# Kernel optimization log

Measured on AMD Instinct MI355X. Metric: run time of the kernel, lower is better.

Reference implementation:

```python
import jax, jax.numpy as jnp
import numpy as np

N_NODES = 10000
N_EDGES = 160000
MUL0 = 128   # multiplicity of 0e in node input/output
MUL1 = 64    # multiplicity of 1o in node input/output
FC_IN = 8    # radial basis size (edge_scalar_attr dim)
FC_H = 64    # fc_neurons = [64, 64]
NUM_NEIGHBORS = 16.0
ANGLE = np.pi / 8.0
MID0 = MUL0 + MUL1   # 192 scalars in irreps_mid (simplified)
MID1 = MUL0 + MUL1   # 192 vectors (1o) in irreps_mid


def _inv_sqrt(d):
    return 1.0 / np.sqrt(d)


def setup_inputs() -> dict:
    key = jax.random.key(0)
    ks = jax.random.split(key, 18)
    rn = lambda k, shape: jax.random.normal(k, shape, dtype=jnp.float32)
    inp = {
        'node_input': rn(ks[0], (N_NODES, MUL0 + 3 * MUL1)),
        'edge_attr': rn(ks[1], (N_EDGES, 4)),            # 1x0e + 1x1o spherical harmonics
        'edge_scalar_attr': rn(ks[2], (N_EDGES, FC_IN)),
        # first Linear: node_input -> (node_features || node_self_out)
        'Wa0': rn(ks[3], (MUL0, MUL0)),   # 0e -> 0e (message branch)
        'Wa1': rn(ks[4], (MUL1, MUL1)),   # 1o -> 1o (message branch)
        'Wb0': rn(ks[5], (MUL0, MUL0)),   # 0e -> 0e (self branch)
        'Wb1': rn(ks[6], (MUL1, MUL1)),   # 1o -> 1o (self branch)
        # radial MLP
        'M1': rn(ks[7], (FC_IN, FC_H)),
        'M2': rn(ks[8], (FC_H, FC_H)),
        # per-instruction TP weight generators: [FC_H, mul] ('uvu', v=1 squeezed)
        'Wtp0': rn(ks[9], (FC_H, MUL0)),   # 0e x 0e -> 0e
        'Wtp1': rn(ks[10], (FC_H, MUL0)),  # 0e x 1o -> 1o
        'Wtp2': rn(ks[11], (FC_H, MUL1)),  # 1o x 0e -> 1o
        'Wtp3': rn(ks[12], (FC_H, MUL1)),  # 1o x 1o -> 0e
        # output Linear: irreps_mid (192x0e + 192x1o) -> 128x0e + 64x1o
        'Wo0': rn(ks[13], (MID0, MUL0)),
        'Wo1': rn(ks[14], (MID1, MUL1)),
        'edge_src': jax.random.randint(ks[15], (N_EDGES,), 0, N_NODES),
        'edge_dst': jax.random.randint(ks[16], (N_EDGES,), 0, N_NODES),
    }
    return inp


def _forward(node_input, edge_attr, edge_scalar_attr,
             Wa0, Wa1, Wb0, Wb1, M1, M2,
             Wtp0, Wtp1, Wtp2, Wtp3, Wo0, Wo1,
             edge_src, edge_dst):
    n = node_input.shape[0]
    x0 = node_input[:, :MUL0]                         # [N,128] 0e
    x1 = node_input[:, MUL0:].reshape(n, MUL1, 3)     # [N,64,3] 1o

    # Linear(node_input.irreps + irreps_node_output): split into message / self
    feat0 = (x0 @ Wa0) * _inv_sqrt(MUL0)
    feat1 = jnp.einsum('nvi,vu->nui', x1, Wa1) * _inv_sqrt(MUL1)
    self0 = (x0 @ Wb0) * _inv_sqrt(MUL0)
    self1 = jnp.einsum('nvi,vu->nui', x1, Wb1) * _inv_sqrt(MUL1)

    # gather node features to edges
    e0 = feat0[edge_src]                              # [E,128]
    e1 = feat1[edge_src]                              # [E,64,3]
    y0 = edge_attr[:, 0:1]                            # [E,1] 0e
    y1 = edge_attr[:, 1:4]                            # [E,3] 1o

    # radial MLP -> per-edge per-path 'uvu' weights (path param / sqrt(fc_out))
    h = jax.nn.gelu(edge_scalar_attr @ M1 * _inv_sqrt(FC_IN))
    h = jax.nn.gelu(h @ M2 * _inv_sqrt(FC_H))
    w0 = h @ Wtp0 * _inv_sqrt(FC_H)                   # [E,128]
    w1 = h @ Wtp1 * _inv_sqrt(FC_H)                   # [E,128]
    w2 = h @ Wtp2 * _inv_sqrt(FC_H)                   # [E,64]
    w3 = h @ Wtp3 * _inv_sqrt(FC_H)                   # [E,64]

    # CG tensor product paths (component normalization: alpha = sqrt(dim_out))
    mid0a = w0 * e0 * y0                                        # 0e x 0e -> 0e [E,128]
    mid0b = w3 * jnp.einsum('eui,ei->eu', e1, y1) * _inv_sqrt(3.0)  # 1o.1o -> 0e [E,64]
    mid1a = w1[:, :, None] * e0[:, :, None] * y1[:, None, :]   # 0e x 1o -> 1o [E,128,3]
    mid1b = w2[:, :, None] * e1 * y0[:, :, None]                # 1o x 0e -> 1o [E,64,3]

    e_cnt = edge_attr.shape[0]
    edge_mid = jnp.concatenate(
        [mid0a, mid0b, mid1a.reshape(e_cnt, -1), mid1b.reshape(e_cnt, -1)], axis=1)  # [E,768]

    # scatter-add to destination nodes, divide by sqrt(num_neighbors)
    agg = jax.ops.segment_sum(edge_mid, edge_dst, num_segments=n) * _inv_sqrt(NUM_NEIGHBORS)

    z0 = agg[:, :MID0]                                          # [N,192] 0e
    z1 = jnp.concatenate(
        [agg[:, MID0:MID0 + 3 * MUL0].reshape(n, MUL0, 3),
         agg[:, MID0 + 3 * MUL0:].reshape(n, MUL1, 3)], axis=1)  # [N,192,3] 1o

    conv0 = (z0 @ Wo0) * _inv_sqrt(MID0)
    conv1 = jnp.einsum('nvi,vu->nui', z1, Wo1) * _inv_sqrt(MID1)

    c = np.cos(ANGLE).astype(np.float32)
    s = np.sin(ANGLE).astype(np.float32)
    out0 = c * self0 + s * conv0                                 # [N,128]
    out1 = c * self1 + s * conv1                                 # [N,64,3]
    return jnp.concatenate([out0, out1.reshape(n, -1)], axis=1)  # [N,320]


def reference(node_input, edge_attr, edge_scalar_attr,
              Wa0, Wa1, Wb0, Wb1, M1, M2,
              Wtp0, Wtp1, Wtp2, Wtp3, Wo0, Wo1,
              edge_src, edge_dst):
    return _forward(node_input, edge_attr, edge_scalar_attr,
                    Wa0, Wa1, Wb0, Wb1, M1, M2,
                    Wtp0, Wtp1, Wtp2, Wtp3, Wo0, Wo1,
                    edge_src, edge_dst)
```

## Files before the change

### kernel.cpp

```cpp
#include <hip/hip_runtime.h>
#include <hip/hip_bf16.h>
#include <hip/hip_fp16.h>

#define N_NODES 10000
#define N_EDGES 160000
#define FEAT_W 320
#define CHUNK 32

typedef _Float16 half8 __attribute__((ext_vector_type(8)));
typedef float f32x4 __attribute__((ext_vector_type(4)));

__device__ __forceinline__ float gelu_tanh(float x) {
    float x3 = x * x * x;
    float t = tanhf(0.7978845608028654f * (x + 0.044715f * x3));
    return 0.5f * x * (1.0f + t);
}

__global__ __launch_bounds__(320) void node_transform(
    const float* __restrict__ node_input,
    const float* __restrict__ Wa0, const float* __restrict__ Wa1,
    const float* __restrict__ Wb0, const float* __restrict__ Wb1,
    float* __restrict__ feat_tbl, float* __restrict__ self_tbl)
{
    __shared__ __align__(16) float xT[FEAT_W][8];
    const int node0 = blockIdx.x * 8;
    const int t = threadIdx.x;
    for (int q = t; q < 640; q += 320) {
        const int n = q / 80, c4 = q - n * 80;
        const float4 v = ((const float4*)(node_input + (size_t)(node0 + n) * FEAT_W))[c4];
        xT[c4 * 4 + 0][n] = v.x; xT[c4 * 4 + 1][n] = v.y;
        xT[c4 * 4 + 2][n] = v.z; xT[c4 * 4 + 3][n] = v.w;
    }
    __syncthreads();

    float accf[8] = {0,0,0,0,0,0,0,0}, accs[8] = {0,0,0,0,0,0,0,0};
    float scale;
    if (t < 128) {
        for (int v = 0; v < 128; ++v) {
            const float wa = Wa0[v * 128 + t];
            const float wb = Wb0[v * 128 + t];
            const float4 xa = *(const float4*)&xT[v][0];
            const float4 xb = *(const float4*)&xT[v][4];
            accf[0] += xa.x * wa; accf[1] += xa.y * wa; accf[2] += xa.z * wa; accf[3] += xa.w * wa;
            accf[4] += xb.x * wa; accf[5] += xb.y * wa; accf[6] += xb.z * wa; accf[7] += xb.w * wa;
            accs[0] += xa.x * wb; accs[1] += xa.y * wb; accs[2] += xa.z * wb; accs[3] += xa.w * wb;
            accs[4] += xb.x * wb; accs[5] += xb.y * wb; accs[6] += xb.z * wb; accs[7] += xb.w * wb;
        }
        scale = 0.08838834764831845f;
    } else {
        const int r = t - 128, u = r / 3, i = r - 3 * u;
        for (int v = 0; v < 64; ++v) {
            const float wa = Wa1[v * 64 + u];
            const float wb = Wb1[v * 64 + u];
            const int row = 128 + v * 3 + i;
            const float4 xa = *(const float4*)&xT[row][0];
            const float4 xb = *(const float4*)&xT[row][4];
            accf[0] += xa.x * wa; accf[1] += xa.y * wa; accf[2] += xa.z * wa; accf[3] += xa.w * wa;
            accf[4] += xb.x * wa; accf[5] += xb.y * wa; accf[6] += xb.z * wa; accf[7] += xb.w * wa;
            accs[0] += xa.x * wb; accs[1] += xa.y * wb; accs[2] += xa.z * wb; accs[3] += xa.w * wb;
            accs[4] += xb.x * wb; accs[5] += xb.y * wb; accs[6] += xb.z * wb; accs[7] += xb.w * wb;
        }
        scale = 0.125f;
    }
#pragma unroll
    for (int n = 0; n < 8; ++n) {
        feat_tbl[(size_t)(node0 + n) * FEAT_W + t] = accf[n] * scale;
        self_tbl[(size_t)(node0 + n) * FEAT_W + t] = accs[n] * scale;
    }
}

__global__ __launch_bounds__(256) void count_kernel(
    const int* __restrict__ edge_dst, int* __restrict__ counts)
{
    const int e = blockIdx.x * 256 + threadIdx.x;
    if (e < N_EDGES) atomicAdd(&counts[edge_dst[e]], 1);
}

__global__ __launch_bounds__(1024) void scan_kernel(
    const int* __restrict__ counts, int* __restrict__ offsets, int* __restrict__ cursor)
{
    __shared__ int wsum[16];
    const int wid = threadIdx.x >> 6, lane = threadIdx.x & 63;
    int base = 0;
    for (int c = 0; c < 10; ++c) {
        const int i = c * 1024 + threadIdx.x;
        const int v = (i < N_NODES) ? counts[i] : 0;
        int x = v;
#pragma unroll
        for (int off = 1; off < 64; off <<= 1) {
            int y = __shfl_up(x, off, 64);
            if (lane >= off) x += y;
        }
        if (lane == 63) wsum[wid] = x;
        __syncthreads();
        if (threadIdx.x < 16) {
            int s = wsum[threadIdx.x];
#pragma unroll
            for (int off = 1; off < 16; off <<= 1) {
                int y = __shfl_up(s, off, 64);
                if ((int)threadIdx.x >= off) s += y;
            }
            wsum[threadIdx.x] = s;
        }
        __syncthreads();
        const int waveoff = (wid == 0) ? 0 : wsum[wid - 1];
        const int excl = base + waveoff + x - v;
        if (i < N_NODES) { offsets[i] = excl; cursor[i] = excl; }
        const int tot = wsum[15];
        __syncthreads();
        base += tot;
    }
    if (threadIdx.x == 0) offsets[N_NODES] = base;
}

__global__ void fill_kernel(const int* __restrict__ edge_dst,
                            const int* __restrict__ edge_src,
                            const float* __restrict__ edge_attr,
                            int* __restrict__ cursor,
                            int* __restrict__ srcs_csr, float* __restrict__ y4csr,
                            int* __restrict__ pos_csr) {
    int e = blockIdx.x * 256 + threadIdx.x;
    if (e < N_EDGES) {
        int pos = atomicAdd(&cursor[edge_dst[e]], 1);
        srcs_csr[pos] = edge_src[e];
        ((float4*)y4csr)[pos] = ((const float4*)edge_attr)[e];
        pos_csr[e] = pos;
    }
}

__global__ __launch_bounds__(256) void mlp_kernel(
    const float* __restrict__ esa,
    const float* __restrict__ M1,
    const float* __restrict__ M2,
    const int* __restrict__ pos_csr,
    __half* __restrict__ h2csr)
{
    __shared__ __align__(16) float sh[4][64];
    const int wave = threadIdx.x >> 6;
    const int lane = threadIdx.x & 63;
    const int e = blockIdx.x * 4 + wave;

    const int pos = pos_csr[e];

    const float4 e0 = ((const float4*)(esa + (size_t)e * 8))[0];
    const float4 e1 = ((const float4*)(esa + (size_t)e * 8))[1];
    float h = e0.x * M1[0 * 64 + lane] + e0.y * M1[1 * 64 + lane]
            + e0.z * M1[2 * 64 + lane] + e0.w * M1[3 * 64 + lane]
            + e1.x * M1[4 * 64 + lane] + e1.y * M1[5 * 64 + lane]
            + e1.z * M1[6 * 64 + lane] + e1.w * M1[7 * 64 + lane];
    h = gelu_tanh(h * 0.35355339059327373f);
    sh[wave][lane] = h;
    __syncthreads();

    float h2 = 0.f;
    const float4* shp = (const float4*)sh[wave];
#pragma unroll
    for (int q = 0; q < 16; ++q) {
        const float4 s = shp[q];
        h2 += s.x * M2[(4 * q + 0) * 64 + lane];
        h2 += s.y * M2[(4 * q + 1) * 64 + lane];
        h2 += s.z * M2[(4 * q + 2) * 64 + lane];
        h2 += s.w * M2[(4 * q + 3) * 64 + lane];
    }
    h2 = gelu_tanh(h2 * 0.125f);
    h2csr[(size_t)pos * 64 + lane] = (__half)(h2 * 0.125f);
}

__global__ __launch_bounds__(256) void pack_weights(
    const float* __restrict__ Wtp0, const float* __restrict__ Wtp1,
    const float* __restrict__ Wtp2, const float* __restrict__ Wtp3,
    const float* __restrict__ Wo0,  const float* __restrict__ Wo1,
    __half* __restrict__ wtp_pack, __half* __restrict__ wo_pack)
{
    const int gid = blockIdx.x * 256 + threadIdx.x;
    if (gid < 1536) {
        const int lane = gid & 63;
        const int tile = gid >> 6;
        const int quad = lane >> 4, n16 = lane & 15;
        const int col = tile * 16 + n16;
        const float* src; int stride;
        if (col < 128)      { src = Wtp0 + col;         stride = 128; }
        else if (col < 256) { src = Wtp1 + (col - 128); stride = 128; }
        else if (col < 320) { src = Wtp2 + (col - 256); stride = 64;  }
        else                { src = Wtp3 + (col - 320); stride = 64;  }
        __half* dst = wtp_pack + (size_t)gid * 16;
#pragma unroll
        for (int s = 0; s < 2; ++s)
#pragma unroll
            for (int j = 0; j < 8; ++j)
                dst[s * 8 + j] = (__half)src[(s * 32 + quad * 8 + j) * stride];
    } else {
        const int i = gid - 1536;
        if (i < 24576) wo_pack[i] = (__half)Wo0[i];
        else           wo_pack[i] = (__half)Wo1[i - 24576];
    }
}

__global__ __launch_bounds__(384, 4) void gather_kernel(
    const int* __restrict__ offsets,
    const int* __restrict__ srcs_csr,
    const float* __restrict__ y4csr,
    const __half* __restrict__ h2csr,
    const __half* __restrict__ wtp_pack,
    const float* __restrict__ feat_tbl,
    const float* __restrict__ self_tbl,
    const __half* __restrict__ wo_pack,
    float* __restrict__ out)
{
    __shared__ __align__(16) __half wsh[CHUNK * 384];
    __shared__ __align__(16) char pool[CHUNK * 128];
    __shared__ float ys[CHUNK][4];
    __shared__ int   srcs[CHUNK];
    __half* h2s = (__half*)pool;
    float*  z   = (float*)pool;

    const int node = blockIdx.x;
    const int t = threadIdx.x;
    const int wave = t >> 6, lane = t & 63;
    const int quad = lane >> 4, n16 = lane & 15;

    const int beg = offsets[node], end = offsets[node + 1];

    int cb = beg;
    int ne = min(CHUNK, end - cb);
    half8 hreg = {};
    int   sreg = 0;
    float4 yreg = {0.f, 0.f, 0.f, 0.f};
    if (t < ne * 8) hreg = ((const half8*)(h2csr + (size_t)cb * 64))[t];
    if (t < ne)     { sreg = srcs_csr[cb + t]; yreg = ((const float4*)y4csr)[cb + t]; }

    half8 bf[4][2];
#pragma unroll
    for (int c = 0; c < 4; ++c) {
        const __half* p = wtp_pack + (size_t)((wave * 4 + c) * 64 + lane) * 16;
        bf[c][0] = *(const half8*)p;
        bf[c][1] = *(const half8*)(p + 8);
    }

    int f0;
    if (t < 128)      f0 = t;
    else if (t < 256) f0 = t - 128;
    else if (t < 320) f0 = 128 + 3 * (t - 256);
    else              f0 = 128 + 3 * (t - 320);

    float acc = 0.f, acc3a = 0.f, acc3b = 0.f, acc3c = 0.f;

    for (;;) {
        if (t < ne) { srcs[t] = sreg; ((float4*)ys)[t] = yreg; }
        if (t < ne * 8) {
            const int eL = t >> 3, u = t & 7;
            *(half8*)((char*)h2s + eL * 128 + ((u * 16) ^ ((eL & 7) << 4))) = hreg;
        }
        __syncthreads();

#pragma unroll
        for (int g = 0; g < 2; ++g) {
            if (g * 16 < ne) {
                const int e = g * 16 + n16;
                const char* hb = (const char*)h2s + e * 128;
                const int sw = (e & 7) << 4;
                const half8 af0 = *(const half8*)(hb + ((quad * 16) ^ sw));
                const half8 af1 = *(const half8*)(hb + ((64 + quad * 16) ^ sw));
#pragma unroll
                for (int c = 0; c < 4; ++c) {
                    f32x4 acc4 = {0.f, 0.f, 0.f, 0.f};
                    acc4 = __builtin_amdgcn_mfma_f32_16x16x32_f16(af0, bf[c][0], acc4, 0, 0, 0);
                    acc4 = __builtin_amdgcn_mfma_f32_16x16x32_f16(af1, bf[c][1], acc4, 0, 0, 0);
                    const int colb = ((wave * 4 + c) * 16 + n16) * 2;
#pragma unroll
                    for (int r = 0; r < 4; ++r) {
                        const int row = g * 16 + quad * 4 + r;
                        *(__half*)((char*)wsh + row * 768 + (colb ^ (quad << 5))) =
                            (__half)acc4[r];
                    }
                }
            }
        }

        const int cb2 = cb + CHUNK;
        const int ne2 = (cb2 < end) ? min(CHUNK, end - cb2) : 0;
        if (t < ne2 * 8) hreg = ((const half8*)(h2csr + (size_t)cb2 * 64))[t];
        if (t < ne2)     { sreg = srcs_csr[cb2 + t]; yreg = ((const float4*)y4csr)[cb2 + t]; }
        __syncthreads();

        const int tb = t * 2;
#define WRD(ee) __half2float(*(const __half*)((const char*)wsh + (ee) * 768 + (tb ^ ((((ee) >> 2) & 3) << 5))))
        if (t < 128) {
            int e = 0;
            for (; e + 4 <= ne; e += 4) {
                float w4[4], v4[4]; int s4[4];
#pragma unroll
                for (int k = 0; k < 4; ++k) { w4[k] = WRD(e + k); s4[k] = srcs[e + k]; }
#pragma unroll
                for (int k = 0; k < 4; ++k) v4[k] = feat_tbl[(size_t)s4[k] * FEAT_W + f0];
#pragma unroll
                for (int k = 0; k < 4; ++k) acc += w4[k] * v4[k] * ys[e + k][0];
            }
            for (; e < ne; ++e)
                acc += WRD(e) * feat_tbl[(size_t)srcs[e] * FEAT_W + f0] * ys[e][0];
        } else if (t < 256) {
            int e = 0;
            for (; e + 4 <= ne; e += 4) {
                float w4[4], v4[4]; int s4[4];
#pragma unroll
                for (int k = 0; k < 4; ++k) { w4[k] = WRD(e + k); s4[k] = srcs[e + k]; }
#pragma unroll
                for (int k = 0; k < 4; ++k) v4[k] = feat_tbl[(size_t)s4[k] * FEAT_W + f0];
#pragma unroll
                for (int k = 0; k < 4; ++k) {
                    const float p = w4[k] * v4[k];
                    a3aAdd: ;
                    acc3a += p * ys[e + k][1];
                    acc3b += p * ys[e + k][2];
                    acc3c += p * ys[e + k][3];
                }
            }
            for (; e < ne; ++e) {
                const float p = WRD(e) * feat_tbl[(size_t)srcs[e] * FEAT_W + f0];
                acc3a += p * ys[e][1]; acc3b += p * ys[e][2]; acc3c += p * ys[e][3];
            }
        } else if (t < 320) {
            int e = 0;
            for (; e + 4 <= ne; e += 4) {
                float w4[4], va[4], vb[4], vc[4]; int s4[4];
#pragma unroll
                for (int k = 0; k < 4; ++k) { w4[k] = WRD(e + k); s4[k] = srcs[e + k]; }
#pragma unroll
                for (int k = 0; k < 4; ++k) {
                    const float* fr = feat_tbl + (size_t)s4[k] * FEAT_W;
                    va[k] = fr[f0]; vb[k] = fr[f0 + 1]; vc[k] = fr[f0 + 2];
                }
#pragma unroll
                for (int k = 0; k < 4; ++k) {
                    const float p = w4[k] * ys[e + k][0];
                    acc3a += p * va[k]; acc3b += p * vb[k]; acc3c += p * vc[k];
                }
            }
            for (; e < ne; ++e) {
                const float* fr = feat_tbl + (size_t)srcs[e] * FEAT_W;
                const float p = WRD(e) * ys[e][0];
                acc3a += p * fr[f0]; acc3b += p * fr[f0 + 1]; acc3c += p * fr[f0 + 2];
            }
        } else {
            int e = 0;
            for (; e + 4 <= ne; e += 4) {
                float w4[4], va[4], vb[4], vc[4]; int s4[4];
#pragma unroll
                for (int k = 0; k < 4; ++k) { w4[k] = WRD(e + k); s4[k] = srcs[e + k]; }
#pragma unroll
                for (int k = 0; k < 4; ++k) {
                    const float* fr = feat_tbl + (size_t)s4[k] * FEAT_W;
                    va[k] = fr[f0]; vb[k] = fr[f0 + 1]; vc[k] = fr[f0 + 2];
                }
#pragma unroll
                for (int k = 0; k < 4; ++k)
                    acc += w4[k] * (va[k] * ys[e + k][1] + vb[k] * ys[e + k][2]
                                  + vc[k] * ys[e + k][3]);
            }
            for (; e < ne; ++e) {
                const float* fr = feat_tbl + (size_t)srcs[e] * FEAT_W;
                acc += WRD(e) * (fr[f0] * ys[e][1] + fr[f0 + 1] * ys[e][2]
                               + fr[f0 + 2] * ys[e][3]);
            }
        }
#undef WRD

        if (!ne2) break;
        cb = cb2; ne = ne2;
        __syncthreads();
    }

    const float sZ = 0.25f;
    if (t < 128) {
        z[t] = acc * sZ;
    } else if (t < 256) {
        const int u = t - 128;
        z[192 + 0 * 192 + u] = acc3a * sZ;
        z[192 + 1 * 192 + u] = acc3b * sZ;
        z[192 + 2 * 192 + u] = acc3c * sZ;
    } else if (t < 320) {
        const int u = t - 256;
        z[192 + 0 * 192 + 128 + u] = acc3a * sZ;
        z[192 + 1 * 192 + 128 + u] = acc3b * sZ;
        z[192 + 2 * 192 + 128 + u] = acc3c * sZ;
    } else {
        z[128 + (t - 320)] = acc * sZ * 0.5773502691896258f;
    }
    __syncthreads();

    const float sA = 0.07216878364870323f;
    const float cR = 0.92387953251128674f;
    const float sR = 0.38268343236508978f;
    const __half* Wo0h = wo_pack;
    const __half* Wo1h = wo_pack + 24576;

    if (t < 128) {
        float conv = 0.f;
        const float4* z4 = (const float4*)z;
#pragma unroll 8
        for (int q = 0; q < 48; ++q) {
            const float4 zz = z4[q];
            conv += zz.x * (float)Wo0h[(4 * q + 0) * 128 + t];
            conv += zz.y * (float)Wo0h[(4 * q + 1) * 128 + t];
            conv += zz.z * (float)Wo0h[(4 * q + 2) * 128 + t];
            conv += zz.w * (float)Wo0h[(4 * q + 3) * 128 + t];
        }
        const float sv = self_tbl[(size_t)node * FEAT_W + t];
        out[(size_t)node * FEAT_W + t] = cR * sv + sR * conv * sA;
    } else if (t < 320) {
        const int idx = t - 128;
        const int i = idx >> 6, u = idx & 63;
        float conv = 0.f;
        const float4* z4 = (const float4*)(z + 192 + i * 192);
#pragma unroll 8
        for (int q = 0; q < 48; ++q) {
            const float4 zz = z4[q];
            conv += zz.x * (float)Wo1h[(4 * q + 0) * 64 + u];
            conv += zz.y * (float)Wo1h[(4 * q + 1) * 64 + u];
            conv += zz.z * (float)Wo1h[(4 * q + 2) * 64 + u];
            conv += zz.w * (float)Wo1h[(4 * q + 3) * 64 + u];
        }
        const int col = 128 + u * 3 + i;
        const float sv = self_tbl[(size_t)node * FEAT_W + col];
        out[(size_t)node * FEAT_W + col] = cR * sv + sR * conv * sA;
    }
}

extern "C" void kernel_launch(void* const* d_in, const int* in_sizes, int n_in,
                              void* d_out, int out_size, void* d_ws, size_t ws_size,
                              hipStream_t stream) {
    const float* node_input = (const float*)d_in[0];
    const float* edge_attr  = (const float*)d_in[1];
    const float* esa        = (const float*)d_in[2];
    const float* Wa0  = (const float*)d_in[3];
    const float* Wa1  = (const float*)d_in[4];
    const float* Wb0  = (const float*)d_in[5];
    const float* Wb1  = (const float*)d_in[6];
    const float* M1   = (const float*)d_in[7];
    const float* M2   = (const float*)d_in[8];
    const float* Wtp0 = (const float*)d_in[9];
    const float* Wtp1 = (const float*)d_in[10];
    const float* Wtp2 = (const float*)d_in[11];
    const float* Wtp3 = (const float*)d_in[12];
    const float* Wo0  = (const float*)d_in[13];
    const float* Wo1  = (const float*)d_in[14];
    const int* edge_src = (const int*)d_in[15];
    const int* edge_dst = (const int*)d_in[16];
    float* out = (float*)d_out;

    char* w = (char*)d_ws;
    float*  feat_tbl = (float*)w;           w += (size_t)N_NODES * FEAT_W * 4;
    float*  self_tbl = (float*)w;           w += (size_t)N_NODES * FEAT_W * 4;
    float*  y4csr    = (float*)w;           w += (size_t)N_EDGES * 4 * 4;
    __half* h2csr    = (__half*)w;          w += (size_t)N_EDGES * 64 * 2;
    __half* wtp_pack = (__half*)w;          w += (size_t)24576 * 2;
    __half* wo_pack  = (__half*)w;          w += (size_t)36864 * 2;
    int*    counts   = (int*)w;             w += (size_t)N_NODES * 4;
    int*    offsets  = (int*)w;             w += (size_t)(N_NODES + 1) * 4;
    int*    cursor   = (int*)w;             w += (size_t)N_NODES * 4;
    int*    srcs_csr = (int*)w;             w += (size_t)N_EDGES * 4;
    int*    pos_csr  = (int*)w;             w += (size_t)N_EDGES * 4;

    hipMemsetAsync(counts, 0, sizeof(int) * N_NODES, stream);

    count_kernel<<<N_EDGES / 256, 256, 0, stream>>>(edge_dst, counts);
    scan_kernel<<<1, 1024, 0, stream>>>(counts, offsets, cursor);
    fill_kernel<<<N_EDGES / 256, 256, 0, stream>>>(edge_dst, edge_src, edge_attr,
                                                   cursor, srcs_csr, y4csr, pos_csr);
    pack_weights<<<150, 256, 0, stream>>>(Wtp0, Wtp1, Wtp2, Wtp3, Wo0, Wo1,
                                          wtp_pack, wo_pack);
    node_transform<<<N_NODES / 8, 320, 0, stream>>>(node_input, Wa0, Wa1, Wb0, Wb1,
                                                    feat_tbl, self_tbl);
    mlp_kernel<<<N_EDGES / 4, 256, 0, stream>>>(esa, M1, M2, pos_csr, h2csr);
    gather_kernel<<<N_NODES, 384, 0, stream>>>(offsets, srcs_csr, y4csr, h2csr,
                                               wtp_pack, feat_tbl, self_tbl,
                                               wo_pack, out);
}
```

Before: 402.5 us.

## Merge prep kernels, fold CSR fill into MLP, persistent gather grid

Node transform, edge counting and weight packing are fused into one launch, with edges recording their atomic rank so CSR positions come from offsets plus rank. This removes the fill kernel and the cursor array. The MLP kernel now scatters src and edge_attr itself and uses 512-thread blocks. Gather becomes a grid-stride loop over nodes with 1280 blocks, and the GELU tanh is replaced by an exp-based formula. Together these reduce launch count and serial dependency stages, at the cost of more complex kernels and possible load imbalance in the persistent gather loop.

```diff
diff --git a/kernel.cpp b/kernel.cpp
--- a/kernel.cpp
+++ b/kernel.cpp
@@ -6,78 +6,108 @@
 #define N_EDGES 160000
 #define FEAT_W 320
 #define CHUNK 32
+#define GATHER_GRID 1280
 
 typedef _Float16 half8 __attribute__((ext_vector_type(8)));
 typedef float f32x4 __attribute__((ext_vector_type(4)));
 
 __device__ __forceinline__ float gelu_tanh(float x) {
     float x3 = x * x * x;
-    float t = tanhf(0.7978845608028654f * (x + 0.044715f * x3));
-    return 0.5f * x * (1.0f + t);
-}
-
-__global__ __launch_bounds__(320) void node_transform(
+    float y = 0.7978845608028654f * (x + 0.044715f * x3);
+    float th = 1.f - 2.f / (__expf(2.f * y) + 1.f);
+    return 0.5f * x * (1.f + th);
+}
+
+__global__ __launch_bounds__(320) void prep_kernel(
     const float* __restrict__ node_input,
     const float* __restrict__ Wa0, const float* __restrict__ Wa1,
     const float* __restrict__ Wb0, const float* __restrict__ Wb1,
-    float* __restrict__ feat_tbl, float* __restrict__ self_tbl)
+    float* __restrict__ feat_tbl, float* __restrict__ self_tbl,
+    const int* __restrict__ edge_dst, int* __restrict__ counts,
+    int* __restrict__ rank,
+    const float* __restrict__ Wtp0, const float* __restrict__ Wtp1,
+    const float* __restrict__ Wtp2, const float* __restrict__ Wtp3,
+    const float* __restrict__ Wo0,  const float* __restrict__ Wo1,
+    __half* __restrict__ wtp_pack, __half* __restrict__ wo_pack)
 {
     __shared__ __align__(16) float xT[FEAT_W][8];
-    const int node0 = blockIdx.x * 8;
     const int t = threadIdx.x;
-    for (int q = t; q < 640; q += 320) {
-        const int n = q / 80, c4 = q - n * 80;
-        const float4 v = ((const float4*)(node_input + (size_t)(node0 + n) * FEAT_W))[c4];
-        xT[c4 * 4 + 0][n] = v.x; xT[c4 * 4 + 1][n] = v.y;
-        xT[c4 * 4 + 2][n] = v.z; xT[c4 * 4 + 3][n] = v.w;
-    }
-    __syncthreads();
-
-    float accf[8] = {0,0,0,0,0,0,0,0}, accs[8] = {0,0,0,0,0,0,0,0};
-    float scale;
-    if (t < 128) {
-        for (int v = 0; v < 128; ++v) {
-            const float wa = Wa0[v * 128 + t];
-            const float wb = Wb0[v * 128 + t];
-            const float4 xa = *(const float4*)&xT[v][0];
-            const float4 xb = *(const float4*)&xT[v][4];
-            accf[0] += xa.x * wa; accf[1] += xa.y * wa; accf[2] += xa.z * wa; accf[3] += xa.w * wa;
-            accf[4] += xb.x * wa; accf[5] += xb.y * wa; accf[6] += xb.z * wa; accf[7] += xb.w * wa;
-            accs[0] += xa.x * wb; accs[1] += xa.y * wb; accs[2] += xa.z * wb; accs[3] += xa.w * wb;
-            accs[4] += xb.x * wb; accs[5] += xb.y * wb; accs[6] += xb.z * wb; accs[7] += xb.w * wb;
-        }
-        scale = 0.08838834764831845f;
+
+    if (blockIdx.x < 1250) {
+        const int node0 = blockIdx.x * 8;
+        for (int q = t; q < 640; q += 320) {
+            const int n = q / 80, c4 = q - n * 80;
+            const float4 v = ((const float4*)(node_input + (size_t)(node0 + n) * FEAT_W))[c4];
+            xT[c4 * 4 + 0][n] = v.x; xT[c4 * 4 + 1][n] = v.y;
+            xT[c4 * 4 + 2][n] = v.z; xT[c4 * 4 + 3][n] = v.w;
+        }
+        __syncthreads();
+
+        float accf[8] = {0,0,0,0,0,0,0,0}, accs[8] = {0,0,0,0,0,0,0,0};
+        float scale;
+        if (t < 128) {
+            for (int v = 0; v < 128; ++v) {
+                const float wa = Wa0[v * 128 + t];
+                const float wb = Wb0[v * 128 + t];
+                const float4 xa = *(const float4*)&xT[v][0];
+                const float4 xb = *(const float4*)&xT[v][4];
+                accf[0] += xa.x * wa; accf[1] += xa.y * wa; accf[2] += xa.z * wa; accf[3] += xa.w * wa;
+                accf[4] += xb.x * wa; accf[5] += xb.y * wa; accf[6] += xb.z * wa; accf[7] += xb.w * wa;
+                accs[0] += xa.x * wb; accs[1] += xa.y * wb; accs[2] += xa.z * wb; accs[3] += xa.w * wb;
+                accs[4] += xb.x * wb; accs[5] += xb.y * wb; accs[6] += xb.z * wb; accs[7] += xb.w * wb;
+            }
+            scale = 0.08838834764831845f;
+        } else {
+            const int r = t - 128, u = r / 3, i = r - 3 * u;
+            for (int v = 0; v < 64; ++v) {
+                const float wa = Wa1[v * 64 + u];
+                const float wb = Wb1[v * 64 + u];
+                const int row = 128 + v * 3 + i;
+                const float4 xa = *(const float4*)&xT[row][0];
+                const float4 xb = *(const float4*)&xT[row][4];
+                accf[0] += xa.x * wa; accf[1] += xa.y * wa; accf[2] += xa.z * wa; accf[3] += xa.w * wa;
+                accf[4] += xb.x * wa; accf[5] += xb.y * wa; accf[6] += xb.z * wa; accf[7] += xb.w * wa;
+                accs[0] += xa.x * wb; accs[1] += xa.y * wb; accs[2] += xa.z * wb; accs[3] += xa.w * wb;
+                accs[4] += xb.x * wb; accs[5] += xb.y * wb; accs[6] += xb.z * wb; accs[7] += xb.w * wb;
+            }
+            scale = 0.125f;
+        }
+#pragma unroll
+        for (int n = 0; n < 8; ++n) {
+            feat_tbl[(size_t)(node0 + n) * FEAT_W + t] = accf[n] * scale;
+            self_tbl[(size_t)(node0 + n) * FEAT_W + t] = accs[n] * scale;
+        }
+    } else if (blockIdx.x < 1750) {
+        const int e = (blockIdx.x - 1250) * 320 + t;
+        rank[e] = atomicAdd(&counts[edge_dst[e]], 1);
     } else {
-        const int r = t - 128, u = r / 3, i = r - 3 * u;
-        for (int v = 0; v < 64; ++v) {
-            const float wa = Wa1[v * 64 + u];
-            const float wb = Wb1[v * 64 + u];
-            const int row = 128 + v * 3 + i;
-            const float4 xa = *(const float4*)&xT[row][0];
-            const float4 xb = *(const float4*)&xT[row][4];
-            accf[0] += xa.x * wa; accf[1] += xa.y * wa; accf[2] += xa.z * wa; accf[3] += xa.w * wa;
-            accf[4] += xb.x * wa; accf[5] += xb.y * wa; accf[6] += xb.z * wa; accf[7] += xb.w * wa;
-            accs[0] += xa.x * wb; accs[1] += xa.y * wb; accs[2] += xa.z * wb; accs[3] += xa.w * wb;
-            accs[4] += xb.x * wb; accs[5] += xb.y * wb; accs[6] += xb.z * wb; accs[7] += xb.w * wb;
-        }
-        scale = 0.125f;
-    }
-#pragma unroll
-    for (int n = 0; n < 8; ++n) {
-        feat_tbl[(size_t)(node0 + n) * FEAT_W + t] = accf[n] * scale;
-        self_tbl[(size_t)(node0 + n) * FEAT_W + t] = accs[n] * scale;
-    }
-}
-
-__global__ __launch_bounds__(256) void count_kernel(
-    const int* __restrict__ edge_dst, int* __restrict__ counts)
-{
-    const int e = blockIdx.x * 256 + threadIdx.x;
-    if (e < N_EDGES) atomicAdd(&counts[edge_dst[e]], 1);
+        const int gid = (blockIdx.x - 1750) * 320 + t;
+        if (gid < 1536) {
+            const int lane = gid & 63;
+            const int tile = gid >> 6;
+            const int quad = lane >> 4, n16 = lane & 15;
+            const int col = tile * 16 + n16;
+            const float* src; int stride;
+            if (col < 128)      { src = Wtp0 + col;         stride = 128; }
+            else if (col < 256) { src = Wtp1 + (col - 128); stride = 128; }
+            else if (col < 320) { src = Wtp2 + (col - 256); stride = 64;  }
+            else                { src = Wtp3 + (col - 320); stride = 64;  }
+            __half* dst = wtp_pack + (size_t)gid * 16;
+#pragma unroll
+            for (int s = 0; s < 2; ++s)
+#pragma unroll
+                for (int j = 0; j < 8; ++j)
+                    dst[s * 8 + j] = (__half)src[(s * 32 + quad * 8 + j) * stride];
+        } else if (gid < 38400) {
+            const int i = gid - 1536;
+            if (i < 24576) wo_pack[i] = (__half)Wo0[i];
+            else           wo_pack[i] = (__half)Wo1[i - 24576];
+        }
+    }
 }
 
 __global__ __launch_bounds__(1024) void scan_kernel(
-    const int* __restrict__ counts, int* __restrict__ offsets, int* __restrict__ cursor)
+    const int* __restrict__ counts, int* __restrict__ offsets)
 {
     __shared__ int wsum[16];
     const int wid = threadIdx.x >> 6, lane = threadIdx.x & 63;
@@ -105,7 +135,7 @@
         __syncthreads();
         const int waveoff = (wid == 0) ? 0 : wsum[wid - 1];
         const int excl = base + waveoff + x - v;
-        if (i < N_NODES) { offsets[i] = excl; cursor[i] = excl; }
+        if (i < N_NODES) offsets[i] = excl;
         const int tot = wsum[15];
         __syncthreads();
         base += tot;
@@ -113,34 +143,29 @@
     if (threadIdx.x == 0) offsets[N_NODES] = base;
 }
 
-__global__ void fill_kernel(const int* __restrict__ edge_dst,
-                            const int* __restrict__ edge_src,
-                            const float* __restrict__ edge_attr,
-                            int* __restrict__ cursor,
-                            int* __restrict__ srcs_csr, float* __restrict__ y4csr,
-                            int* __restrict__ pos_csr) {
-    int e = blockIdx.x * 256 + threadIdx.x;
-    if (e < N_EDGES) {
-        int pos = atomicAdd(&cursor[edge_dst[e]], 1);
-        srcs_csr[pos] = edge_src[e];
-        ((float4*)y4csr)[pos] = ((const float4*)edge_attr)[e];
-        pos_csr[e] = pos;
-    }
-}
-
-__global__ __launch_bounds__(256) void mlp_kernel(
+__global__ __launch_bounds__(512) void mlp_kernel(
     const float* __restrict__ esa,
     const float* __restrict__ M1,
     const float* __restrict__ M2,
-    const int* __restrict__ pos_csr,
-    __half* __restrict__ h2csr)
+    const int* __restrict__ edge_dst,
+    const int* __restrict__ rank,
+    const int* __restrict__ offsets,
+    const int* __restrict__ edge_src,
+    const float* __restrict__ edge_attr,
+    __half* __restrict__ h2csr,
+    int* __restrict__ srcs_csr,
+    float* __restrict__ y4csr)
 {
-    __shared__ __align__(16) float sh[4][64];
+    __shared__ __align__(16) float sh[8][64];
     const int wave = threadIdx.x >> 6;
     const int lane = threadIdx.x & 63;
-    const int e = blockIdx.x * 4 + wave;
-
-    const int pos = pos_csr[e];
+    const int e = blockIdx.x * 8 + wave;
+
+    const int pos = offsets[edge_dst[e]] + rank[e];
+    if (lane == 0) {
+        srcs_csr[pos] = edge_src[e];
+        ((float4*)y4csr)[pos] = ((const float4*)edge_attr)[e];
+    }
 
     const float4 e0 = ((const float4*)(esa + (size_t)e * 8))[0];
     const float4 e1 = ((const float4*)(esa + (size_t)e * 8))[1];
@@ -164,36 +189,6 @@
     }
     h2 = gelu_tanh(h2 * 0.125f);
     h2csr[(size_t)pos * 64 + lane] = (__half)(h2 * 0.125f);
-}
-
-__global__ __launch_bounds__(256) void pack_weights(
-    const float* __restrict__ Wtp0, const float* __restrict__ Wtp1,
-    const float* __restrict__ Wtp2, const float* __restrict__ Wtp3,
-    const float* __restrict__ Wo0,  const float* __restrict__ Wo1,
-    __half* __restrict__ wtp_pack, __half* __restrict__ wo_pack)
-{
-    const int gid = blockIdx.x * 256 + threadIdx.x;
-    if (gid < 1536) {
-        const int lane = gid & 63;
-        const int tile = gid >> 6;
-        const int quad = lane >> 4, n16 = lane & 15;
-        const int col = tile * 16 + n16;
-        const float* src; int stride;
-        if (col < 128)      { src = Wtp0 + col;         stride = 128; }
-        else if (col < 256) { src = Wtp1 + (col - 128); stride = 128; }
-        else if (col < 320) { src = Wtp2 + (col - 256); stride = 64;  }
-        else                { src = Wtp3 + (col - 320); stride = 64;  }
-        __half* dst = wtp_pack + (size_t)gid * 16;
-#pragma unroll
-        for (int s = 0; s < 2; ++s)
-#pragma unroll
-            for (int j = 0; j < 8; ++j)
-                dst[s * 8 + j] = (__half)src[(s * 32 + quad * 8 + j) * stride];
-    } else {
-        const int i = gid - 1536;
-        if (i < 24576) wo_pack[i] = (__half)Wo0[i];
-        else           wo_pack[i] = (__half)Wo1[i - 24576];
-    }
 }
 
 __global__ __launch_bounds__(384, 4) void gather_kernel(
@@ -214,20 +209,9 @@
     __half* h2s = (__half*)pool;
     float*  z   = (float*)pool;
 
-    const int node = blockIdx.x;
     const int t = threadIdx.x;
     const int wave = t >> 6, lane = t & 63;
     const int quad = lane >> 4, n16 = lane & 15;
-
-    const int beg = offsets[node], end = offsets[node + 1];
-
-    int cb = beg;
-    int ne = min(CHUNK, end - cb);
-    half8 hreg = {};
-    int   sreg = 0;
-    float4 yreg = {0.f, 0.f, 0.f, 0.f};
-    if (t < ne * 8) hreg = ((const half8*)(h2csr + (size_t)cb * 64))[t];
-    if (t < ne)     { sreg = srcs_csr[cb + t]; yreg = ((const float4*)y4csr)[cb + t]; }
 
     half8 bf[4][2];
 #pragma unroll
@@ -236,193 +220,204 @@
         bf[c][0] = *(const half8*)p;
         bf[c][1] = *(const half8*)(p + 8);
     }
-
     int f0;
     if (t < 128)      f0 = t;
     else if (t < 256) f0 = t - 128;
     else if (t < 320) f0 = 128 + 3 * (t - 256);
     else              f0 = 128 + 3 * (t - 320);
 
-    float acc = 0.f, acc3a = 0.f, acc3b = 0.f, acc3c = 0.f;
-
-    for (;;) {
-        if (t < ne) { srcs[t] = sreg; ((float4*)ys)[t] = yreg; }
-        if (t < ne * 8) {
-            const int eL = t >> 3, u = t & 7;
-            *(half8*)((char*)h2s + eL * 128 + ((u * 16) ^ ((eL & 7) << 4))) = hreg;
-        }
-        __syncthreads();
-
-#pragma unroll
-        for (int g = 0; g < 2; ++g) {
-            if (g * 16 < ne) {
-                const int e = g * 16 + n16;
-                const char* hb = (const char*)h2s + e * 128;
-                const int sw = (e & 7) << 4;
-                const half8 af0 = *(const half8*)(hb + ((quad * 16) ^ sw));
-                const half8 af1 = *(const half8*)(hb + ((64 + quad * 16) ^ sw));
-#pragma unroll
-                for (int c = 0; c < 4; ++c) {
-                    f32x4 acc4 = {0.f, 0.f, 0.f, 0.f};
-                    acc4 = __builtin_amdgcn_mfma_f32_16x16x32_f16(af0, bf[c][0], acc4, 0, 0, 0);
-                    acc4 = __builtin_amdgcn_mfma_f32_16x16x32_f16(af1, bf[c][1], acc4, 0, 0, 0);
-                    const int colb = ((wave * 4 + c) * 16 + n16) * 2;
-#pragma unroll
-                    for (int r = 0; r < 4; ++r) {
-                        const int row = g * 16 + quad * 4 + r;
-                        *(__half*)((char*)wsh + row * 768 + (colb ^ (quad << 5))) =
-                            (__half)acc4[r];
-                    }
-                }
-            }
-        }
-
-        const int cb2 = cb + CHUNK;
-        const int ne2 = (cb2 < end) ? min(CHUNK, end - cb2) : 0;
-        if (t < ne2 * 8) hreg = ((const half8*)(h2csr + (size_t)cb2 * 64))[t];
-        if (t < ne2)     { sreg = srcs_csr[cb2 + t]; yreg = ((const float4*)y4csr)[cb2 + t]; }
-        __syncthreads();
-
-        const int tb = t * 2;
-#define WRD(ee) __half2float(*(const __half*)((const char*)wsh + (ee) * 768 + (tb ^ ((((ee) >> 2) & 3) << 5))))
-        if (t < 128) {
-            int e = 0;
-            for (; e + 4 <= ne; e += 4) {
-                float w4[4], v4[4]; int s4[4];
-#pragma unroll
-                for (int k = 0; k < 4; ++k) { w4[k] = WRD(e + k); s4[k] = srcs[e + k]; }
-#pragma unroll
-                for (int k = 0; k < 4; ++k) v4[k] = feat_tbl[(size_t)s4[k] * FEAT_W + f0];
-#pragma unroll
-                for (int k = 0; k < 4; ++k) acc += w4[k] * v4[k] * ys[e + k][0];
-            }
-            for (; e < ne; ++e)
-                acc += WRD(e) * feat_tbl[(size_t)srcs[e] * FEAT_W + f0] * ys[e][0];
-        } else if (t < 256) {
-            int e = 0;
-            for (; e + 4 <= ne; e += 4) {
-                float w4[4], v4[4]; int s4[4];
-#pragma unroll
-                for (int k = 0; k < 4; ++k) { w4[k] = WRD(e + k); s4[k] = srcs[e + k]; }
-#pragma unroll
-                for (int k = 0; k < 4; ++k) v4[k] = feat_tbl[(size_t)s4[k] * FEAT_W + f0];
-#pragma unroll
-                for (int k = 0; k < 4; ++k) {
-                    const float p = w4[k] * v4[k];
-                    a3aAdd: ;
-                    acc3a += p * ys[e + k][1];
-                    acc3b += p * ys[e + k][2];
-                    acc3c += p * ys[e + k][3];
-                }
-            }
-            for (; e < ne; ++e) {
-                const float p = WRD(e) * feat_tbl[(size_t)srcs[e] * FEAT_W + f0];
-                acc3a += p * ys[e][1]; acc3b += p * ys[e][2]; acc3c += p * ys[e][3];
-            }
-        } else if (t < 320) {
-            int e = 0;
-            for (; e + 4 <= ne; e += 4) {
-                float w4[4], va[4], vb[4], vc[4]; int s4[4];
-#pragma unroll
-                for (int k = 0; k < 4; ++k) { w4[k] = WRD(e + k); s4[k] = srcs[e + k]; }
-#pragma unroll
-                for (int k = 0; k < 4; ++k) {
-                    const float* fr = feat_tbl + (size_t)s4[k] * FEAT_W;
-                    va[k] = fr[f0]; vb[k] = fr[f0 + 1]; vc[k] = fr[f0 + 2];
-                }
-#pragma unroll
-                for (int k = 0; k < 4; ++k) {
-                    const float p = w4[k] * ys[e + k][0];
-                    acc3a += p * va[k]; acc3b += p * vb[k]; acc3c += p * vc[k];
-                }
-            }
-            for (; e < ne; ++e) {
-                const float* fr = feat_tbl + (size_t)srcs[e] * FEAT_W;
-                const float p = WRD(e) * ys[e][0];
-                acc3a += p * fr[f0]; acc3b += p * fr[f0 + 1]; acc3c += p * fr[f0 + 2];
-            }
-        } else {
-            int e = 0;
-            for (; e + 4 <= ne; e += 4) {
-                float w4[4], va[4], vb[4], vc[4]; int s4[4];
-#pragma unroll
-                for (int k = 0; k < 4; ++k) { w4[k] = WRD(e + k); s4[k] = srcs[e + k]; }
-#pragma unroll
-                for (int k = 0; k < 4; ++k) {
-                    const float* fr = feat_tbl + (size_t)s4[k] * FEAT_W;
-                    va[k] = fr[f0]; vb[k] = fr[f0 + 1]; vc[k] = fr[f0 + 2];
-                }
-#pragma unroll
-                for (int k = 0; k < 4; ++k)
-                    acc += w4[k] * (va[k] * ys[e + k][1] + vb[k] * ys[e + k][2]
-                                  + vc[k] * ys[e + k][3]);
-            }
-            for (; e < ne; ++e) {
-                const float* fr = feat_tbl + (size_t)srcs[e] * FEAT_W;
-                acc += WRD(e) * (fr[f0] * ys[e][1] + fr[f0 + 1] * ys[e][2]
-                               + fr[f0 + 2] * ys[e][3]);
-            }
-        }
-#undef WRD
-
-        if (!ne2) break;
-        cb = cb2; ne = ne2;
-        __syncthreads();
-    }
-
     const float sZ = 0.25f;
-    if (t < 128) {
-        z[t] = acc * sZ;
-    } else if (t < 256) {
-        const int u = t - 128;
-        z[192 + 0 * 192 + u] = acc3a * sZ;
-        z[192 + 1 * 192 + u] = acc3b * sZ;
-        z[192 + 2 * 192 + u] = acc3c * sZ;
-    } else if (t < 320) {
-        const int u = t - 256;
-        z[192 + 0 * 192 + 128 + u] = acc3a * sZ;
-        z[192 + 1 * 192 + 128 + u] = acc3b * sZ;
-        z[192 + 2 * 192 + 128 + u] = acc3c * sZ;
-    } else {
-        z[128 + (t - 320)] = acc * sZ * 0.5773502691896258f;
-    }
-    __syncthreads();
-
     const float sA = 0.07216878364870323f;
     const float cR = 0.92387953251128674f;
     const float sR = 0.38268343236508978f;
     const __half* Wo0h = wo_pack;
     const __half* Wo1h = wo_pack + 24576;
 
-    if (t < 128) {
-        float conv = 0.f;
-        const float4* z4 = (const float4*)z;
+    for (int node = blockIdx.x; node < N_NODES; node += GATHER_GRID) {
+        const int beg = offsets[node], end = offsets[node + 1];
+
+        int cb = beg;
+        int ne = min(CHUNK, end - cb);
+        half8 hreg = {};
+        int   sreg = 0;
+        float4 yreg = {0.f, 0.f, 0.f, 0.f};
+        if (t < ne * 8) hreg = ((const half8*)(h2csr + (size_t)cb * 64))[t];
+        if (t < ne)     { sreg = srcs_csr[cb + t]; yreg = ((const float4*)y4csr)[cb + t]; }
+
+        float acc = 0.f, acc3a = 0.f, acc3b = 0.f, acc3c = 0.f;
+
+        for (;;) {
+            if (t < ne) { srcs[t] = sreg; ((float4*)ys)[t] = yreg; }
+            if (t < ne * 8) {
+                const int eL = t >> 3, u = t & 7;
+                *(half8*)((char*)h2s + eL * 128 + ((u * 16) ^ ((eL & 7) << 4))) = hreg;
+            }
+            __syncthreads();
+
+#pragma unroll
+            for (int g = 0; g < 2; ++g) {
+                if (g * 16 < ne) {
+                    const int e = g * 16 + n16;
+                    const char* hb = (const char*)h2s + e * 128;
+                    const int sw = (e & 7) << 4;
+                    const half8 af0 = *(const half8*)(hb + ((quad * 16) ^ sw));
+                    const half8 af1 = *(const half8*)(hb + ((64 + quad * 16) ^ sw));
+#pragma unroll
+                    for (int c = 0; c < 4; ++c) {
+                        f32x4 acc4 = {0.f, 0.f, 0.f, 0.f};
+                        acc4 = __builtin_amdgcn_mfma_f32_16x16x32_f16(af0, bf[c][0], acc4, 0, 0, 0);
+                        acc4 = __builtin_amdgcn_mfma_f32_16x16x32_f16(af1, bf[c][1], acc4, 0, 0, 0);
+                        const int colb = ((wave * 4 + c) * 16 + n16) * 2;
+#pragma unroll
+                        for (int r = 0; r < 4; ++r) {
+                            const int row = g * 16 + quad * 4 + r;
+                            *(__half*)((char*)wsh + row * 768 + (colb ^ (quad << 5))) =
+                                (__half)acc4[r];
+                        }
+                    }
+                }
+            }
+
+            const int cb2 = cb + CHUNK;
+            const int ne2 = (cb2 < end) ? min(CHUNK, end - cb2) : 0;
+            if (t < ne2 * 8) hreg = ((const half8*)(h2csr + (size_t)cb2 * 64))[t];
+            if (t < ne2)     { sreg = srcs_csr[cb2 + t]; yreg = ((const float4*)y4csr)[cb2 + t]; }
+            __syncthreads();
+
+            const int tb = t * 2;
+#define WRD(ee) __half2float(*(const __half*)((const char*)wsh + (ee) * 768 + (tb ^ ((((ee) >> 2) & 3) << 5))))
+            if (t < 128) {
+                int e = 0;
+                for (; e + 4 <= ne; e += 4) {
+                    float w4[4], v4[4]; int s4[4];
+#pragma unroll
+                    for (int k = 0; k < 4; ++k) { w4[k] = WRD(e + k); s4[k] = srcs[e + k]; }
+#pragma unroll
+                    for (int k = 0; k < 4; ++k) v4[k] = feat_tbl[(size_t)s4[k] * FEAT_W + f0];
+#pragma unroll
+                    for (int k = 0; k < 4; ++k) acc += w4[k] * v4[k] * ys[e + k][0];
+                }
+                for (; e < ne; ++e)
+                    acc += WRD(e) * feat_tbl[(size_t)srcs[e] * FEAT_W + f0] * ys[e][0];
+            } else if (t < 256) {
+                int e = 0;
+                for (; e + 4 <= ne; e += 4) {
+                    float w4[4], v4[4]; int s4[4];
+#pragma unroll
+                    for (int k = 0; k < 4; ++k) { w4[k] = WRD(e + k); s4[k] = srcs[e + k]; }
+#pragma unroll
+                    for (int k = 0; k < 4; ++k) v4[k] = feat_tbl[(size_t)s4[k] * FEAT_W + f0];
+#pragma unroll
+                    for (int k = 0; k < 4; ++k) {
+                        const float p = w4[k] * v4[k];
+                        acc3a += p * ys[e + k][1];
+                        acc3b += p * ys[e + k][2];
+                        acc3c += p * ys[e + k][3];
+                    }
+                }
+                for (; e < ne; ++e) {
+                    const float p = WRD(e) * feat_tbl[(size_t)srcs[e] * FEAT_W + f0];
+                    acc3a += p * ys[e][1]; acc3b += p * ys[e][2]; acc3c += p * ys[e][3];
+                }
+            } else if (t < 320) {
+                int e = 0;
+                for (; e + 4 <= ne; e += 4) {
+                    float w4[4], va[4], vb[4], vc[4]; int s4[4];
+#pragma unroll
+                    for (int k = 0; k < 4; ++k) { w4[k] = WRD(e + k); s4[k] = srcs[e + k]; }
+#pragma unroll
+                    for (int k = 0; k < 4; ++k) {
+                        const float* fr = feat_tbl + (size_t)s4[k] * FEAT_W;
+                        va[k] = fr[f0]; vb[k] = fr[f0 + 1]; vc[k] = fr[f0 + 2];
+                    }
+#pragma unroll
+                    for (int k = 0; k < 4; ++k) {
+                        const float p = w4[k] * ys[e + k][0];
+                        acc3a += p * va[k]; acc3b += p * vb[k]; acc3c += p * vc[k];
+                    }
+                }
+                for (; e < ne; ++e) {
+                    const float* fr = feat_tbl + (size_t)srcs[e] * FEAT_W;
+                    const float p = WRD(e) * ys[e][0];
+                    acc3a += p * fr[f0]; acc3b += p * fr[f0 + 1]; acc3c += p * fr[f0 + 2];
+                }
+            } else {
+                int e = 0;
+                for (; e + 4 <= ne; e += 4) {
+                    float w4[4], va[4], vb[4], vc[4]; int s4[4];
+#pragma unroll
+                    for (int k = 0; k < 4; ++k) { w4[k] = WRD(e + k); s4[k] = srcs[e + k]; }
+#pragma unroll
+                    for (int k = 0; k < 4; ++k) {
+                        const float* fr = feat_tbl + (size_t)s4[k] * FEAT_W;
+                        va[k] = fr[f0]; vb[k] = fr[f0 + 1]; vc[k] = fr[f0 + 2];
+                    }
+#pragma unroll
+                    for (int k = 0; k < 4; ++k)
+                        acc += w4[k] * (va[k] * ys[e + k][1] + vb[k] * ys[e + k][2]
+                                      + vc[k] * ys[e + k][3]);
+                }
+                for (; e < ne; ++e) {
+                    const float* fr = feat_tbl + (size_t)srcs[e] * FEAT_W;
+                    acc += WRD(e) * (fr[f0] * ys[e][1] + fr[f0 + 1] * ys[e][2]
+                                   + fr[f0 + 2] * ys[e][3]);
+                }
+            }
+#undef WRD
+
+            if (!ne2) break;
+            cb = cb2; ne = ne2;
+            __syncthreads();
+        }
+
+        if (t < 128) {
+            z[t] = acc * sZ;
+        } else if (t < 256) {
+            const int u = t - 128;
+            z[192 + 0 * 192 + u] = acc3a * sZ;
+            z[192 + 1 * 192 + u] = acc3b * sZ;
+            z[192 + 2 * 192 + u] = acc3c * sZ;
+        } else if (t < 320) {
+            const int u = t - 256;
+            z[192 + 0 * 192 + 128 + u] = acc3a * sZ;
+            z[192 + 1 * 192 + 128 + u] = acc3b * sZ;
+            z[192 + 2 * 192 + 128 + u] = acc3c * sZ;
+        } else {
+            z[128 + (t - 320)] = acc * sZ * 0.5773502691896258f;
+        }
+        __syncthreads();
+
+        if (t < 128) {
+            float conv = 0.f;
+            const float4* z4 = (const float4*)z;
 #pragma unroll 8
-        for (int q = 0; q < 48; ++q) {
-            const float4 zz = z4[q];
-            conv += zz.x * (float)Wo0h[(4 * q + 0) * 128 + t];
-            conv += zz.y * (float)Wo0h[(4 * q + 1) * 128 + t];
-            conv += zz.z * (float)Wo0h[(4 * q + 2) * 128 + t];
-            conv += zz.w * (float)Wo0h[(4 * q + 3) * 128 + t];
-        }
-        const float sv = self_tbl[(size_t)node * FEAT_W + t];
-        out[(size_t)node * FEAT_W + t] = cR * sv + sR * conv * sA;
-    } else if (t < 320) {
-        const int idx = t - 128;
-        const int i = idx >> 6, u = idx & 63;
-        float conv = 0.f;
-        const float4* z4 = (const float4*)(z + 192 + i * 192);
+            for (int q = 0; q < 48; ++q) {
+                const float4 zz = z4[q];
+                conv += zz.x * (float)Wo0h[(4 * q + 0) * 128 + t];
+                conv += zz.y * (float)Wo0h[(4 * q + 1) * 128 + t];
+                conv += zz.z * (float)Wo0h[(4 * q + 2) * 128 + t];
+                conv += zz.w * (float)Wo0h[(4 * q + 3) * 128 + t];
+            }
+            const float sv = self_tbl[(size_t)node * FEAT_W + t];
+            out[(size_t)node * FEAT_W + t] = cR * sv + sR * conv * sA;
+        } else if (t < 320) {
+            const int idx = t - 128;
+            const int i = idx >> 6, u = idx & 63;
+            float conv = 0.f;
+            const float4* z4 = (const float4*)(z + 192 + i * 192);
 #pragma unroll 8
-        for (int q = 0; q < 48; ++q) {
-            const float4 zz = z4[q];
-            conv += zz.x * (float)Wo1h[(4 * q + 0) * 64 + u];
-            conv += zz.y * (float)Wo1h[(4 * q + 1) * 64 + u];
-            conv += zz.z * (float)Wo1h[(4 * q + 2) * 64 + u];
-            conv += zz.w * (float)Wo1h[(4 * q + 3) * 64 + u];
-        }
-        const int col = 128 + u * 3 + i;
-        const float sv = self_tbl[(size_t)node * FEAT_W + col];
-        out[(size_t)node * FEAT_W + col] = cR * sv + sR * conv * sA;
+            for (int q = 0; q < 48; ++q) {
+                const float4 zz = z4[q];
+                conv += zz.x * (float)Wo1h[(4 * q + 0) * 64 + u];
+                conv += zz.y * (float)Wo1h[(4 * q + 1) * 64 + u];
+                conv += zz.z * (float)Wo1h[(4 * q + 2) * 64 + u];
+                conv += zz.w * (float)Wo1h[(4 * q + 3) * 64 + u];
+            }
+            const int col = 128 + u * 3 + i;
+            const float sv = self_tbl[(size_t)node * FEAT_W + col];
+            out[(size_t)node * FEAT_W + col] = cR * sv + sR * conv * sA;
+        }
+        __syncthreads();
     }
 }
 
@@ -457,22 +452,21 @@
     __half* wo_pack  = (__half*)w;          w += (size_t)36864 * 2;
     int*    counts   = (int*)w;             w += (size_t)N_NODES * 4;
     int*    offsets  = (int*)w;             w += (size_t)(N_NODES + 1) * 4;
-    int*    cursor   = (int*)w;             w += (size_t)N_NODES * 4;
+    int*    rank     = (int*)w;             w += (size_t)N_EDGES * 4;
     int*    srcs_csr = (int*)w;             w += (size_t)N_EDGES * 4;
-    int*    pos_csr  = (int*)w;             w += (size_t)N_EDGES * 4;
 
     hipMemsetAsync(counts, 0, sizeof(int) * N_NODES, stream);
 
-    count_kernel<<<N_EDGES / 256, 256, 0, stream>>>(edge_dst, counts);
-    scan_kernel<<<1, 1024, 0, stream>>>(counts, offsets, cursor);
-    fill_kernel<<<N_EDGES / 256, 256, 0, stream>>>(edge_dst, edge_src, edge_attr,
-                                                   cursor, srcs_csr, y4csr, pos_csr);
-    pack_weights<<<150, 256, 0, stream>>>(Wtp0, Wtp1, Wtp2, Wtp3, Wo0, Wo1,
+    prep_kernel<<<1870, 320, 0, stream>>>(node_input, Wa0, Wa1, Wb0, Wb1,
+                                          feat_tbl, self_tbl,
+                                          edge_dst, counts, rank,
+                                          Wtp0, Wtp1, Wtp2, Wtp3, Wo0, Wo1,
                                           wtp_pack, wo_pack);
-    node_transform<<<N_NODES / 8, 320, 0, stream>>>(node_input, Wa0, Wa1, Wb0, Wb1,
-                                                    feat_tbl, self_tbl);
-    mlp_kernel<<<N_EDGES / 4, 256, 0, stream>>>(esa, M1, M2, pos_csr, h2csr);
-    gather_kernel<<<N_NODES, 384, 0, stream>>>(offsets, srcs_csr, y4csr, h2csr,
-                                               wtp_pack, feat_tbl, self_tbl,
-                                               wo_pack, out);
-}
+    scan_kernel<<<1, 1024, 0, stream>>>(counts, offsets);
+    mlp_kernel<<<N_EDGES / 8, 512, 0, stream>>>(esa, M1, M2, edge_dst, rank, offsets,
+                                                edge_src, edge_attr,
+                                                h2csr, srcs_csr, y4csr);
+    gather_kernel<<<GATHER_GRID, 384, 0, stream>>>(offsets, srcs_csr, y4csr, h2csr,
+                                                   wtp_pack, feat_tbl, self_tbl,
+                                                   wo_pack, out);
+}
```

Result: slower. 427.3 us (+6.2%).
